# Kernel optimization log

Hardware: AMD Instinct MI355X
Metric: run time of the kernel (lower is better)

Reference implementation:

```python
import jax, jax.numpy as jnp
import numpy as np

N = 50000
E = 800000
IN_C, HID_C, OUT_C = 128, 128, 40
K = 3  # PyG TAGConv default number of hops


def setup_inputs() -> dict:
    key = jax.random.key(0)
    k1, k2, k3, k4, k5, k6, k7 = jax.random.split(key, 7)
    x = jax.random.normal(k1, (N, IN_C), dtype=jnp.float32)
    edge_index = jax.random.randint(k2, (2, E), 0, N, dtype=jnp.int64)
    # Linear((K+1)*in, out) weights (stored as [in_total, out] for x @ W)
    s1 = 1.0 / np.sqrt((K + 1) * IN_C)
    s2 = 1.0 / np.sqrt((K + 1) * HID_C)
    W1 = jax.random.uniform(k3, ((K + 1) * IN_C, HID_C), jnp.float32, -s1, s1)
    b1 = jax.random.uniform(k4, (HID_C,), jnp.float32, -s1, s1)
    W2 = jax.random.uniform(k5, ((K + 1) * HID_C, OUT_C), jnp.float32, -s2, s2)
    b2 = jax.random.uniform(k6, (OUT_C,), jnp.float32, -s2, s2)
    return {"x": x, "edge_index": edge_index, "W1": W1, "b1": b1, "W2": W2, "b2": b2}


def _sym_norm(src, dst):
    # GCN-style symmetric normalization: deg computed on destination (col)
    deg = jax.ops.segment_sum(jnp.ones((E,), jnp.float32), dst, num_segments=N)
    dis = jnp.where(deg > 0, jax.lax.rsqrt(jnp.maximum(deg, 1.0)), 0.0)
    return dis[src] * dis[dst]  # [E]


def _tag_layer(x, src, dst, norm, W, b):
    xs = [x]
    h = x
    for _ in range(K):
        h = jax.ops.segment_sum(h[src] * norm[:, None], dst, num_segments=N)
        xs.append(h)
    return jnp.concatenate(xs, axis=1) @ W + b


def reference(x, edge_index, W1, b1, W2, b2):
    src, dst = edge_index[0], edge_index[1]
    norm = _sym_norm(src, dst)
    h = jax.nn.relu(_tag_layer(x, src, dst, norm, W1, b1))
    # F.dropout(training=False) is identity at inference
    h = _tag_layer(h, src, dst, norm, W2, b2)
    return jax.nn.log_softmax(h, axis=1)
```

## Files before the change

kernel.cpp:

```cpp
#include <hip/hip_runtime.h>
#include <hip/hip_bf16.h>

#define NNODES 50000
#define NROWP  50176
#define NEDGES 800000
#define KHOP 3
#define SCAN_NB 49
#define NBKT 196
#define BCAP 6144
#define ABLK 400
#define ACH  2000

typedef __attribute__((ext_vector_type(8))) short short8v;
typedef __attribute__((ext_vector_type(8))) __bf16 bf16x8;
typedef __attribute__((ext_vector_type(4))) float f32x4;

__device__ inline unsigned short f2bf(float f) {
  unsigned u = __builtin_bit_cast(unsigned, f);
  u += 0x7fffu + ((u >> 16) & 1u);
  return (unsigned short)(u >> 16);
}
__device__ inline float bf2f(unsigned short h) {
  return __builtin_bit_cast(float, (unsigned)h << 16);
}
__device__ inline float bflo(unsigned u) { return __builtin_bit_cast(float, u << 16); }
__device__ inline float bfhi(unsigned u) { return __builtin_bit_cast(float, u & 0xffff0000u); }

__device__ inline void gload_lds16(const void* g, void* l) {
  __builtin_amdgcn_global_load_lds(
      (const __attribute__((address_space(1))) unsigned int*)g,
      (__attribute__((address_space(3))) unsigned int*)l, 16, 0, 0);
}

__device__ inline f32x4 mfma_bf16(bf16x8 a, bf16x8 b, f32x4 c) {
  return __builtin_amdgcn_mfma_f32_16x16x32_bf16(a, b, c, 0, 0, 0);
}

__device__ inline void fma8(float* acc, float w, short8v v) {
  uint4 u = __builtin_bit_cast(uint4, v);
  acc[0] = fmaf(w, bflo(u.x), acc[0]);
  acc[1] = fmaf(w, bfhi(u.x), acc[1]);
  acc[2] = fmaf(w, bflo(u.y), acc[2]);
  acc[3] = fmaf(w, bfhi(u.y), acc[3]);
  acc[4] = fmaf(w, bflo(u.z), acc[4]);
  acc[5] = fmaf(w, bfhi(u.z), acc[5]);
  acc[6] = fmaf(w, bflo(u.w), acc[6]);
  acc[7] = fmaf(w, bfhi(u.w), acc[7]);
}

__device__ inline void fma4(float* acc, float w, uint2 v) {
  acc[0] = fmaf(w, bflo(v.x), acc[0]);
  acc[1] = fmaf(w, bfhi(v.x), acc[1]);
  acc[2] = fmaf(w, bflo(v.y), acc[2]);
  acc[3] = fmaf(w, bfhi(v.y), acc[3]);
}

__global__ __launch_bounds__(256) void bucketA_kernel(
    const int* __restrict__ src, const int* __restrict__ dst,
    int* __restrict__ bcur, int2* __restrict__ bkt) {
  __shared__ int2 eb[ACH];
  __shared__ int hist[256];
  __shared__ int base[256];
  int tid = threadIdx.x;
  int e0 = blockIdx.x * ACH;
  int cnt = NEDGES - e0; if (cnt > ACH) cnt = ACH;
  hist[tid] = 0;
  __syncthreads();
  for (int i = tid; i < cnt; i += 256) {
    int s = src[e0 + i], d = dst[e0 + i];
    eb[i] = make_int2(s, d);
    atomicAdd(&hist[d >> 8], 1);
  }
  __syncthreads();
  base[tid] = atomicAdd(&bcur[tid], hist[tid]);
  hist[tid] = 0;
  __syncthreads();
  for (int i = tid; i < cnt; i += 256) {
    int2 e = eb[i];
    int b = e.y >> 8;
    int off = atomicAdd(&hist[b], 1);
    bkt[(size_t)b * BCAP + base[b] + off] = e;
  }
}

__global__ __launch_bounds__(256) void histB_kernel(
    const int* __restrict__ bcur, const int2* __restrict__ bkt,
    int* __restrict__ cnt, int n) {
  __shared__ int h[256];
  int b = blockIdx.x, tid = threadIdx.x;
  h[tid] = 0;
  __syncthreads();
  int sz = bcur[b];
  for (int i = tid; i < sz; i += 256)
    atomicAdd(&h[bkt[(size_t)b * BCAP + i].y & 255], 1);
  __syncthreads();
  int node = b * 256 + tid;
  if (node < n) cnt[node] = h[tid];
}

__global__ __launch_bounds__(256) void bsum_kernel(const int* __restrict__ cnt,
                                                   int* __restrict__ bsums, int n) {
  __shared__ int sd[256];
  int tid = threadIdx.x;
  int base = blockIdx.x * 1024 + tid * 4;
  int s = 0;
  if (base + 4 <= n) {
    int4 v = *(const int4*)&cnt[base];
    s = v.x + v.y + v.z + v.w;
  }
  sd[tid] = s;
  __syncthreads();
  for (int o = 128; o; o >>= 1) {
    if (tid < o) sd[tid] += sd[tid + o];
    __syncthreads();
  }
  if (tid == 0) bsums[blockIdx.x] = sd[0];
}

__global__ __launch_bounds__(64) void bscan_kernel(const int* __restrict__ bsums,
                                                   int* __restrict__ boff,
                                                   int* __restrict__ row_ptr,
                                                   int nb, int n) {
  int tid = threadIdx.x;
  int own = (tid < nb) ? bsums[tid] : 0;
  int v = own;
#pragma unroll
  for (int o = 1; o < 64; o <<= 1) {
    int t = __shfl_up(v, o, 64);
    if (tid >= o) v += t;
  }
  if (tid < nb) boff[tid] = v - own;
  if (tid == 63) row_ptr[n] = v;
}

__global__ __launch_bounds__(256) void bfinal_kernel(const int* __restrict__ cnt,
                                                     const int* __restrict__ boff,
                                                     int* __restrict__ row_ptr,
                                                     float* __restrict__ dis, int n) {
  __shared__ int sd[256];
  int tid = threadIdx.x;
  int base = blockIdx.x * 1024 + tid * 4;
  int4 v = make_int4(0, 0, 0, 0);
  bool ok = (base + 4 <= n);
  if (ok) v = *(const int4*)&cnt[base];
  int s = v.x + v.y + v.z + v.w;
  sd[tid] = s;
  __syncthreads();
  for (int o = 1; o < 256; o <<= 1) {
    int t = (tid >= o) ? sd[tid - o] : 0;
    __syncthreads();
    sd[tid] += t;
    __syncthreads();
  }
  if (ok) {
    int run = boff[blockIdx.x] + sd[tid] - s;
    int4 rp;
    rp.x = run;
    rp.y = run + v.x;
    rp.z = rp.y + v.y;
    rp.w = rp.z + v.z;
    *(int4*)&row_ptr[base] = rp;
    float4 dv;
    dv.x = (v.x > 0) ? rsqrtf((float)v.x) : 0.f;
    dv.y = (v.y > 0) ? rsqrtf((float)v.y) : 0.f;
    dv.z = (v.z > 0) ? rsqrtf((float)v.z) : 0.f;
    dv.w = (v.w > 0) ? rsqrtf((float)v.w) : 0.f;
    *(float4*)&dis[base] = dv;
  }
}

__global__ __launch_bounds__(256) void scatB_kernel(
    const int* __restrict__ bcur, const int2* __restrict__ bkt,
    const int* __restrict__ row_ptr, const float* __restrict__ dis,
    int2* __restrict__ csr, int n) {
  __shared__ int cur[256];
  int b = blockIdx.x, tid = threadIdx.x;
  int node = b * 256 + tid;
  cur[tid] = (node < n) ? row_ptr[node] : 0;
  __syncthreads();
  int sz = bcur[b];
  for (int i = tid; i < sz; i += 256) {
    int2 e = bkt[(size_t)b * BCAP + i];
    int pos = atomicAdd(&cur[e.y & 255], 1);
    int2 ent;
    ent.x = e.x;
    ent.y = __float_as_int(dis[e.x] * dis[e.y]);
    csr[pos] = ent;
  }
}

__global__ void wprep_kernel(const float* __restrict__ W1, const float* __restrict__ W2,
                             unsigned short* __restrict__ W1t,
                             unsigned short* __restrict__ W2pt) {
  int t = blockIdx.x * blockDim.x + threadIdx.x;
  if (t < 512 * 128) {
    int c = t >> 9, k = t & 511;
    W1t[t] = f2bf(W1[(size_t)k * 128 + c]);
  } else if (t < 512 * 128 + 160 * 128) {
    int u = t - 512 * 128;
    int q = u >> 7, r = u & 127;
    int k = q / 40, c = q - k * 40;
    W2pt[u] = f2bf(W2[(size_t)(k * 128 + r) * 40 + c]);
  }
}

__global__ void copyx_kernel(const float* __restrict__ x, unsigned short* __restrict__ P, int n) {
  int t = blockIdx.x * blockDim.x + threadIdx.x;
  int i = t >> 5;
  int c4 = (t & 31) << 2;
  if (i < n) {
    float4 v = *(const float4*)&x[(size_t)i * 128 + c4];
    unsigned lo = (unsigned)f2bf(v.x) | ((unsigned)f2bf(v.y) << 16);
    unsigned hi = (unsigned)f2bf(v.z) | ((unsigned)f2bf(v.w) << 16);
    uint2 o; o.x = lo; o.y = hi;
    *(uint2*)&P[(size_t)i * 512 + c4] = o;
  }
}

__global__ __launch_bounds__(256) void prop128c_kernel(
    const unsigned short* __restrict__ in, unsigned short* __restrict__ out,
    const int* __restrict__ row_ptr, const int2* __restrict__ csr, int n) {
  int node = (int)((blockIdx.x * blockDim.x + threadIdx.x) >> 6);
  int lane = threadIdx.x & 63;
  if (node >= n) return;
  int beg = row_ptr[node], end = row_ptr[node + 1];
  int deg = end - beg;
  int2 ent = make_int2(0, 0);
  if (lane < deg) ent = csr[beg + lane];
  const int grp = lane >> 4, sub = lane & 15;
  float acc[8] = {0.f, 0.f, 0.f, 0.f, 0.f, 0.f, 0.f, 0.f};
  int m = deg < 64 ? deg : 64;
  for (int j = 0; j < m; j += 4) {
    int idx = j + grp;
    bool act = idx < m;
    int ic = act ? idx : m - 1;
    int s = __shfl(ent.x, ic, 64);
    float w = __int_as_float(__shfl(ent.y, ic, 64));
    if (!act) w = 0.f;
    short8v v = *(const short8v*)(in + (size_t)s * 512 + sub * 8);
    fma8(acc, w, v);
  }
  for (int t = beg + 64; t < end; ++t) {
    int2 e0 = csr[t];
    float w = (grp == 0) ? __int_as_float(e0.y) : 0.f;
    short8v v = *(const short8v*)(in + (size_t)e0.x * 512 + sub * 8);
    fma8(acc, w, v);
  }
#pragma unroll
  for (int i = 0; i < 8; ++i) {
    acc[i] += __shfl_xor(acc[i], 16, 64);
    acc[i] += __shfl_xor(acc[i], 32, 64);
  }
  if (grp == 0) {
    uint4 r;
    r.x = (unsigned)f2bf(acc[0]) | ((unsigned)f2bf(acc[1]) << 16);
    r.y = (unsigned)f2bf(acc[2]) | ((unsigned)f2bf(acc[3]) << 16);
    r.z = (unsigned)f2bf(acc[4]) | ((unsigned)f2bf(acc[5]) << 16);
    r.w = (unsigned)f2bf(acc[6]) | ((unsigned)f2bf(acc[7]) << 16);
    *(uint4*)(out + (size_t)node * 512 + sub * 8) = r;
  }
}

__global__ __launch_bounds__(256) void gemm1m_kernel(
    const unsigned short* __restrict__ A,
    const unsigned short* __restrict__ Bt,
    const float* __restrict__ bias,
    unsigned short* __restrict__ H) {
  __shared__ short As[64 * 32];
  __shared__ short Bs[128 * 32];
  const int tid = threadIdx.x;
  const int lane = tid & 63;
  const int w = tid >> 6;
  const int wr = w & 1;
  const int wc = w >> 1;
  const int row0 = blockIdx.x * 64;
  f32x4 acc[2][4];
#pragma unroll
  for (int i = 0; i < 2; ++i)
#pragma unroll
    for (int j = 0; j < 4; ++j) acc[i][j] = (f32x4)0.f;

  const int lrow = lane >> 2;
  const int lkp = lane & 3;

  for (int k0 = 0; k0 < 512; k0 += 32) {
    gload_lds16(A + (size_t)(row0 + w * 16 + lrow) * 512 + k0 + lkp * 8, &As[w * 512]);
    gload_lds16(Bt + (size_t)(w * 16 + lrow) * 512 + k0 + lkp * 8, &Bs[w * 512]);
    gload_lds16(Bt + (size_t)((w + 4) * 16 + lrow) * 512 + k0 + lkp * 8, &Bs[(w + 4) * 512]);
    __syncthreads();
    const int kg = lane >> 4, rr = lane & 15;
    bf16x8 af[2], bfr[4];
#pragma unroll
    for (int mr = 0; mr < 2; ++mr)
      af[mr] = __builtin_bit_cast(bf16x8,
          *(const short8v*)&As[(wr * 32 + mr * 16 + rr) * 32 + kg * 8]);
#pragma unroll
    for (int nr = 0; nr < 4; ++nr)
      bfr[nr] = __builtin_bit_cast(bf16x8,
          *(const short8v*)&Bs[(wc * 64 + nr * 16 + rr) * 32 + kg * 8]);
#pragma unroll
    for (int mr = 0; mr < 2; ++mr)
#pragma unroll
      for (int nr = 0; nr < 4; ++nr)
        acc[mr][nr] = mfma_bf16(af[mr], bfr[nr], acc[mr][nr]);
    __syncthreads();
  }
  const int cg = lane >> 4, cl = lane & 15;
#pragma unroll
  for (int mr = 0; mr < 2; ++mr)
#pragma unroll
    for (int nr = 0; nr < 4; ++nr) {
      int col = wc * 64 + nr * 16 + cl;
      float bv = bias[col];
#pragma unroll
      for (int j = 0; j < 4; ++j) {
        int row = row0 + wr * 32 + mr * 16 + cg * 4 + j;
        H[(size_t)row * 128 + col] = f2bf(fmaxf(acc[mr][nr][j] + bv, 0.f));
      }
    }
}

__global__ __launch_bounds__(256) void gemm2m_kernel(
    const unsigned short* __restrict__ A,
    const unsigned short* __restrict__ Bt,
    unsigned short* __restrict__ G) {
  __shared__ short As[64 * 32];
  __shared__ short Bs[160 * 32];
  const int tid = threadIdx.x;
  const int lane = tid & 63;
  const int w = tid >> 6;
  const int row0 = blockIdx.x * 64;
  f32x4 acc[10];
#pragma unroll
  for (int i = 0; i < 10; ++i) acc[i] = (f32x4)0.f;
  const int lrow = lane >> 2, lkp = lane & 3;

  for (int k0 = 0; k0 < 128; k0 += 32) {
    gload_lds16(A + (size_t)(row0 + w * 16 + lrow) * 128 + k0 + lkp * 8, &As[w * 512]);
    for (int c = w; c < 10; c += 4)
      gload_lds16(Bt + (size_t)(c * 16 + lrow) * 128 + k0 + lkp * 8, &Bs[c * 512]);
    __syncthreads();
    const int kg = lane >> 4, rr = lane & 15;
    bf16x8 af = __builtin_bit_cast(bf16x8,
        *(const short8v*)&As[(w * 16 + rr) * 32 + kg * 8]);
#pragma unroll
    for (int nr = 0; nr < 10; ++nr) {
      bf16x8 bfr = __builtin_bit_cast(bf16x8,
          *(const short8v*)&Bs[(nr * 16 + rr) * 32 + kg * 8]);
      acc[nr] = mfma_bf16(af, bfr, acc[nr]);
    }
    __syncthreads();
  }
  const int cg = lane >> 4, cl = lane & 15;
#pragma unroll
  for (int nr = 0; nr < 10; ++nr) {
    int col = nr * 16 + cl;
    int k = col / 40;
    int o = col - k * 40;
#pragma unroll
    for (int j = 0; j < 4; ++j) {
      int row = row0 + w * 16 + cg * 4 + j;
      G[(size_t)k * NROWP * 64 + (size_t)row * 64 + o] = f2bf(acc[nr][j]);
    }
  }
}

__global__ __launch_bounds__(256) void prop40c_kernel(
    const unsigned short* __restrict__ in,
    const unsigned short* __restrict__ add,
    unsigned short* __restrict__ out,
    const int* __restrict__ row_ptr, const int2* __restrict__ csr, int n) {
  int node = (int)((blockIdx.x * blockDim.x + threadIdx.x) >> 6);
  int lane = threadIdx.x & 63;
  if (node >= n) return;
  int beg = row_ptr[node], end = row_ptr[node + 1];
  int deg = end - beg;
  int2 ent = make_int2(0, 0);
  if (lane < deg) ent = csr[beg + lane];
  const int grp = lane >> 4, sub = lane & 15;
  float acc[4] = {0.f, 0.f, 0.f, 0.f};
  if (grp == 0) {
    uint2 a = *(const uint2*)(add + (size_t)node * 64 + sub * 4);
    acc[0] = bflo(a.x); acc[1] = bfhi(a.x);
    acc[2] = bflo(a.y); acc[3] = bfhi(a.y);
  }
  int m = deg < 64 ? deg : 64;
  for (int j = 0; j < m; j += 4) {
    int idx = j + grp;
    bool act = idx < m;
    int ic = act ? idx : m - 1;
    int s = __shfl(ent.x, ic, 64);
    float w = __int_as_float(__shfl(ent.y, ic, 64));
    if (!act) w = 0.f;
    uint2 v = *(const uint2*)(in + (size_t)s * 64 + sub * 4);
    fma4(acc, w, v);
  }
  for (int t = beg + 64; t < end; ++t) {
    int2 e0 = csr[t];
    float w = (grp == 0) ? __int_as_float(e0.y) : 0.f;
    uint2 v = *(const uint2*)(in + (size_t)e0.x * 64 + sub * 4);
    fma4(acc, w, v);
  }
#pragma unroll
  for (int i = 0; i < 4; ++i) {
    acc[i] += __shfl_xor(acc[i], 16, 64);
    acc[i] += __shfl_xor(acc[i], 32, 64);
  }
  if (grp == 0) {
    uint2 r;
    r.x = (unsigned)f2bf(acc[0]) | ((unsigned)f2bf(acc[1]) << 16);
    r.y = (unsigned)f2bf(acc[2]) | ((unsigned)f2bf(acc[3]) << 16);
    *(uint2*)(out + (size_t)node * 64 + sub * 4) = r;
  }
}

__global__ __launch_bounds__(256) void prop40c_lsm_kernel(
    const unsigned short* __restrict__ in,
    const unsigned short* __restrict__ add,
    const float* __restrict__ b2,
    float* __restrict__ out,
    const int* __restrict__ row_ptr, const int2* __restrict__ csr, int n) {
  int node = (int)((blockIdx.x * blockDim.x + threadIdx.x) >> 6);
  int lane = threadIdx.x & 63;
  if (node >= n) return;
  int beg = row_ptr[node], end = row_ptr[node + 1];
  int deg = end - beg;
  int2 ent = make_int2(0, 0);
  if (lane < deg) ent = csr[beg + lane];
  const int grp = lane >> 4, sub = lane & 15;
  float acc[4] = {0.f, 0.f, 0.f, 0.f};
  if (grp == 0) {
    uint2 a = *(const uint2*)(add + (size_t)node * 64 + sub * 4);
    acc[0] = bflo(a.x); acc[1] = bfhi(a.x);
    acc[2] = bflo(a.y); acc[3] = bfhi(a.y);
  }
  int m = deg < 64 ? deg : 64;
  for (int j = 0; j < m; j += 4) {
    int idx = j + grp;
    bool act = idx < m;
    int ic = act ? idx : m - 1;
    int s = __shfl(ent.x, ic, 64);
    float w = __int_as_float(__shfl(ent.y, ic, 64));
    if (!act) w = 0.f;
    uint2 v = *(const uint2*)(in + (size_t)s * 64 + sub * 4);
    fma4(acc, w, v);
  }
  for (int t = beg + 64; t < end; ++t) {
    int2 e0 = csr[t];
    float w = (grp == 0) ? __int_as_float(e0.y) : 0.f;
    uint2 v = *(const uint2*)(in + (size_t)e0.x * 64 + sub * 4);
    fma4(acc, w, v);
  }
#pragma unroll
  for (int i = 0; i < 4; ++i) {
    acc[i] += __shfl_xor(acc[i], 16, 64);
    acc[i] += __shfl_xor(acc[i], 32, 64);
  }
  bool val = (sub < 10);
  float vv[4];
  if (val) {
    float4 bv = *(const float4*)(b2 + sub * 4);
    vv[0] = acc[0] + bv.x; vv[1] = acc[1] + bv.y;
    vv[2] = acc[2] + bv.z; vv[3] = acc[3] + bv.w;
  } else {
    vv[0] = vv[1] = vv[2] = vv[3] = -__builtin_inff();
  }
  float mx = fmaxf(fmaxf(vv[0], vv[1]), fmaxf(vv[2], vv[3]));
#pragma unroll
  for (int o = 1; o < 16; o <<= 1) mx = fmaxf(mx, __shfl_xor(mx, o, 64));
  float s = 0.f;
  if (val)
    s = expf(vv[0] - mx) + expf(vv[1] - mx) + expf(vv[2] - mx) + expf(vv[3] - mx);
#pragma unroll
  for (int o = 1; o < 16; o <<= 1) s += __shfl_xor(s, o, 64);
  if (val) {
    float ls = logf(s);
    float4 o4;
    o4.x = vv[0] - mx - ls; o4.y = vv[1] - mx - ls;
    o4.z = vv[2] - mx - ls; o4.w = vv[3] - mx - ls;
    *(float4*)(out + (size_t)node * 40 + sub * 4) = o4;
  }
}

extern "C" void kernel_launch(void* const* d_in, const int* in_sizes, int n_in,
                              void* d_out, int out_size, void* d_ws, size_t ws_size,
                              hipStream_t stream) {
  const float* x  = (const float*)d_in[0];
  const int*   ei = (const int*)d_in[1];
  const float* W1 = (const float*)d_in[2];
  const float* b1 = (const float*)d_in[3];
  const float* W2 = (const float*)d_in[4];
  const float* b2 = (const float*)d_in[5];
  const int* srcv = ei;
  const int* dstv = ei + NEDGES;
  float* out = (float*)d_out;

  char* wsb = (char*)d_ws;
  size_t off = 0;
  auto alloc = [&](size_t bytes) {
    char* p = wsb + off;
    off += (bytes + 255) & ~(size_t)255;
    return p;
  };
  int*            cnt     = (int*)            alloc((size_t)NNODES * 4);
  float*          dis     = (float*)          alloc((size_t)NNODES * 4);
  int*            row_ptr = (int*)            alloc(((size_t)NNODES + 1) * 4);
  int*            bcur    = (int*)            alloc((size_t)256 * 4);
  int*            bsums   = (int*)            alloc((size_t)SCAN_NB * 4);
  int*            boff    = (int*)            alloc((size_t)SCAN_NB * 4);
  int2*           bkt     = (int2*)           alloc((size_t)NBKT * BCAP * 8);
  int2*           csr     = (int2*)           alloc((size_t)NEDGES * 8);
  unsigned short* W1t     = (unsigned short*) alloc((size_t)128 * 512 * 2);
  unsigned short* W2pt    = (unsigned short*) alloc((size_t)160 * 128 * 2);
  unsigned short* P       = (unsigned short*) alloc((size_t)NROWP * 512 * 2);
  unsigned short* H       = (unsigned short*) alloc((size_t)NROWP * 128 * 2);
  unsigned short* G       = (unsigned short*) alloc((size_t)4 * NROWP * 64 * 2);
  unsigned short* tb      = (unsigned short*) alloc((size_t)NNODES * 64 * 2);
  unsigned short* t2      = (unsigned short*) alloc((size_t)NNODES * 64 * 2);

  unsigned short* G0 = G;
  unsigned short* G1 = G + (size_t)1 * NROWP * 64;
  unsigned short* G2 = G + (size_t)2 * NROWP * 64;
  unsigned short* G3 = G + (size_t)3 * NROWP * 64;

  hipMemsetAsync(bcur, 0, 256 * 4, stream);
  bucketA_kernel<<<ABLK, 256, 0, stream>>>(srcv, dstv, bcur, bkt);
  histB_kernel<<<NBKT, 256, 0, stream>>>(bcur, bkt, cnt, NNODES);
  bsum_kernel<<<SCAN_NB, 256, 0, stream>>>(cnt, bsums, NNODES);
  bscan_kernel<<<1, 64, 0, stream>>>(bsums, boff, row_ptr, SCAN_NB, NNODES);
  bfinal_kernel<<<SCAN_NB, 256, 0, stream>>>(cnt, boff, row_ptr, dis, NNODES);
  scatB_kernel<<<NBKT, 256, 0, stream>>>(bcur, bkt, row_ptr, dis, csr, NNODES);
  wprep_kernel<<<(512 * 128 + 160 * 128 + 255) / 256, 256, 0, stream>>>(W1, W2, W1t, W2pt);
  copyx_kernel<<<((NNODES * 32) + 255) / 256, 256, 0, stream>>>(x, P, NNODES);

  const int prop_blocks = (NNODES * 64 + 255) / 256;
  for (int k = 1; k <= KHOP; ++k)
    prop128c_kernel<<<prop_blocks, 256, 0, stream>>>(P + 128 * (k - 1), P + 128 * k,
                                                     row_ptr, csr, NNODES);
  const int gemm_blocks = (NNODES + 63) / 64;
  gemm1m_kernel<<<gemm_blocks, 256, 0, stream>>>(P, W1t, b1, H);
  gemm2m_kernel<<<gemm_blocks, 256, 0, stream>>>(H, W2pt, G);
  prop40c_kernel<<<prop_blocks, 256, 0, stream>>>(G3, G2, tb, row_ptr, csr, NNODES);
  prop40c_kernel<<<prop_blocks, 256, 0, stream>>>(tb, G1, t2, row_ptr, csr, NNODES);
  prop40c_lsm_kernel<<<prop_blocks, 256, 0, stream>>>(t2, G0, b2, out, row_ptr, csr, NNODES);
}
```

Before: 254.3 us.

## Split feature matrix into 32-column blocks and map column blocks to XCDs in propagation

Changes the P buffer from row-major 512-wide rows to a blocked layout of 32 bf16 columns per node per block. Each workgroup in the 128-wide propagation now handles one 32-column block for 4 nodes, and the workgroup id is decoded so that each column block lands on a fixed pair of XCDs. The goal is for each XCD's L2 to cache only its slice of the gathered features, which cuts cross-XCD cache duplication in the random neighbor gathers. In exchange there are 4x more workgroups, each doing smaller 8-byte loads, and the neighbor lists are re-read once per column block. The copy and GEMM1 A-operand loads are adapted to the new layout.

```diff
diff --git a/kernel.cpp b/kernel.cpp
--- a/kernel.cpp
+++ b/kernel.cpp
@@ -10,6 +10,7 @@
 #define BCAP 6144
 #define ABLK 400
 #define ACH  2000
+#define PXWG 50000
 
 typedef __attribute__((ext_vector_type(8))) short short8v;
 typedef __attribute__((ext_vector_type(8))) __bf16 bf16x8;
@@ -20,9 +21,6 @@
   u += 0x7fffu + ((u >> 16) & 1u);
   return (unsigned short)(u >> 16);
 }
-__device__ inline float bf2f(unsigned short h) {
-  return __builtin_bit_cast(float, (unsigned)h << 16);
-}
 __device__ inline float bflo(unsigned u) { return __builtin_bit_cast(float, u << 16); }
 __device__ inline float bfhi(unsigned u) { return __builtin_bit_cast(float, u & 0xffff0000u); }
 
@@ -34,18 +32,6 @@
 
 __device__ inline f32x4 mfma_bf16(bf16x8 a, bf16x8 b, f32x4 c) {
   return __builtin_amdgcn_mfma_f32_16x16x32_bf16(a, b, c, 0, 0, 0);
-}
-
-__device__ inline void fma8(float* acc, float w, short8v v) {
-  uint4 u = __builtin_bit_cast(uint4, v);
-  acc[0] = fmaf(w, bflo(u.x), acc[0]);
-  acc[1] = fmaf(w, bfhi(u.x), acc[1]);
-  acc[2] = fmaf(w, bflo(u.y), acc[2]);
-  acc[3] = fmaf(w, bfhi(u.y), acc[3]);
-  acc[4] = fmaf(w, bflo(u.z), acc[4]);
-  acc[5] = fmaf(w, bfhi(u.z), acc[5]);
-  acc[6] = fmaf(w, bflo(u.w), acc[6]);
-  acc[7] = fmaf(w, bfhi(u.w), acc[7]);
 }
 
 __device__ inline void fma4(float* acc, float w, uint2 v) {
@@ -204,60 +190,68 @@
   }
 }
 
-__global__ void copyx_kernel(const float* __restrict__ x, unsigned short* __restrict__ P, int n) {
+__global__ void copyx_kernel(const float* __restrict__ x, unsigned short* __restrict__ Pb, int n) {
   int t = blockIdx.x * blockDim.x + threadIdx.x;
-  int i = t >> 5;
-  int c4 = (t & 31) << 2;
+  int i = t >> 4;
+  int sl = t & 15;
   if (i < n) {
-    float4 v = *(const float4*)&x[(size_t)i * 128 + c4];
-    unsigned lo = (unsigned)f2bf(v.x) | ((unsigned)f2bf(v.y) << 16);
-    unsigned hi = (unsigned)f2bf(v.z) | ((unsigned)f2bf(v.w) << 16);
-    uint2 o; o.x = lo; o.y = hi;
-    *(uint2*)&P[(size_t)i * 512 + c4] = o;
-  }
-}
-
-__global__ __launch_bounds__(256) void prop128c_kernel(
+    int c = sl >> 2, q = sl & 3;
+    float4 v0 = *(const float4*)&x[(size_t)i * 128 + c * 32 + q * 8];
+    float4 v1 = *(const float4*)&x[(size_t)i * 128 + c * 32 + q * 8 + 4];
+    uint4 r;
+    r.x = (unsigned)f2bf(v0.x) | ((unsigned)f2bf(v0.y) << 16);
+    r.y = (unsigned)f2bf(v0.z) | ((unsigned)f2bf(v0.w) << 16);
+    r.z = (unsigned)f2bf(v1.x) | ((unsigned)f2bf(v1.y) << 16);
+    r.w = (unsigned)f2bf(v1.z) | ((unsigned)f2bf(v1.w) << 16);
+    *(uint4*)(Pb + ((size_t)c * NROWP + i) * 32 + q * 8) = r;
+  }
+}
+
+__global__ __launch_bounds__(256) void prop128x_kernel(
     const unsigned short* __restrict__ in, unsigned short* __restrict__ out,
     const int* __restrict__ row_ptr, const int2* __restrict__ csr, int n) {
-  int node = (int)((blockIdx.x * blockDim.x + threadIdx.x) >> 6);
+  int wgid = blockIdx.x;
+  int xcd = wgid & 7;
+  int cb = xcd >> 1;
+  int chunk = (wgid >> 3) * 2 + (xcd & 1);
+  int node = chunk * 4 + (threadIdx.x >> 6);
   int lane = threadIdx.x & 63;
   if (node >= n) return;
   int beg = row_ptr[node], end = row_ptr[node + 1];
   int deg = end - beg;
   int2 ent = make_int2(0, 0);
   if (lane < deg) ent = csr[beg + lane];
-  const int grp = lane >> 4, sub = lane & 15;
-  float acc[8] = {0.f, 0.f, 0.f, 0.f, 0.f, 0.f, 0.f, 0.f};
+  const int slot = lane >> 3, sub = lane & 7;
+  const unsigned short* inb = in + (size_t)cb * NROWP * 32;
+  float acc[4] = {0.f, 0.f, 0.f, 0.f};
   int m = deg < 64 ? deg : 64;
-  for (int j = 0; j < m; j += 4) {
-    int idx = j + grp;
+  for (int j = 0; j < m; j += 8) {
+    int idx = j + slot;
     bool act = idx < m;
     int ic = act ? idx : m - 1;
     int s = __shfl(ent.x, ic, 64);
     float w = __int_as_float(__shfl(ent.y, ic, 64));
     if (!act) w = 0.f;
-    short8v v = *(const short8v*)(in + (size_t)s * 512 + sub * 8);
-    fma8(acc, w, v);
+    uint2 v = *(const uint2*)(inb + (size_t)s * 32 + sub * 4);
+    fma4(acc, w, v);
   }
   for (int t = beg + 64; t < end; ++t) {
     int2 e0 = csr[t];
-    float w = (grp == 0) ? __int_as_float(e0.y) : 0.f;
-    short8v v = *(const short8v*)(in + (size_t)e0.x * 512 + sub * 8);
-    fma8(acc, w, v);
-  }
-#pragma unroll
-  for (int i = 0; i < 8; ++i) {
+    float w = (slot == 0) ? __int_as_float(e0.y) : 0.f;
+    uint2 v = *(const uint2*)(inb + (size_t)e0.x * 32 + sub * 4);
+    fma4(acc, w, v);
+  }
+#pragma unroll
+  for (int i = 0; i < 4; ++i) {
+    acc[i] += __shfl_xor(acc[i], 8, 64);
     acc[i] += __shfl_xor(acc[i], 16, 64);
     acc[i] += __shfl_xor(acc[i], 32, 64);
   }
-  if (grp == 0) {
-    uint4 r;
+  if (slot == 0) {
+    uint2 r;
     r.x = (unsigned)f2bf(acc[0]) | ((unsigned)f2bf(acc[1]) << 16);
     r.y = (unsigned)f2bf(acc[2]) | ((unsigned)f2bf(acc[3]) << 16);
-    r.z = (unsigned)f2bf(acc[4]) | ((unsigned)f2bf(acc[5]) << 16);
-    r.w = (unsigned)f2bf(acc[6]) | ((unsigned)f2bf(acc[7]) << 16);
-    *(uint4*)(out + (size_t)node * 512 + sub * 8) = r;
+    *(uint2*)(out + ((size_t)cb * NROWP + node) * 32 + sub * 4) = r;
   }
 }
 
@@ -284,7 +278,8 @@
   const int lkp = lane & 3;
 
   for (int k0 = 0; k0 < 512; k0 += 32) {
-    gload_lds16(A + (size_t)(row0 + w * 16 + lrow) * 512 + k0 + lkp * 8, &As[w * 512]);
+    const int blk = k0 >> 5;
+    gload_lds16(A + ((size_t)blk * NROWP + row0 + w * 16 + lrow) * 32 + lkp * 8, &As[w * 512]);
     gload_lds16(Bt + (size_t)(w * 16 + lrow) * 512 + k0 + lkp * 8, &Bs[w * 512]);
     gload_lds16(Bt + (size_t)((w + 4) * 16 + lrow) * 512 + k0 + lkp * 8, &Bs[(w + 4) * 512]);
     __syncthreads();
@@ -531,15 +526,16 @@
   bfinal_kernel<<<SCAN_NB, 256, 0, stream>>>(cnt, boff, row_ptr, dis, NNODES);
   scatB_kernel<<<NBKT, 256, 0, stream>>>(bcur, bkt, row_ptr, dis, csr, NNODES);
   wprep_kernel<<<(512 * 128 + 160 * 128 + 255) / 256, 256, 0, stream>>>(W1, W2, W1t, W2pt);
-  copyx_kernel<<<((NNODES * 32) + 255) / 256, 256, 0, stream>>>(x, P, NNODES);
-
-  const int prop_blocks = (NNODES * 64 + 255) / 256;
+  copyx_kernel<<<((NNODES * 16) + 255) / 256, 256, 0, stream>>>(x, P, NNODES);
+
+  const size_t hopstride = (size_t)4 * NROWP * 32;
   for (int k = 1; k <= KHOP; ++k)
-    prop128c_kernel<<<prop_blocks, 256, 0, stream>>>(P + 128 * (k - 1), P + 128 * k,
-                                                     row_ptr, csr, NNODES);
+    prop128x_kernel<<<PXWG, 256, 0, stream>>>(P + hopstride * (k - 1), P + hopstride * k,
+                                              row_ptr, csr, NNODES);
   const int gemm_blocks = (NNODES + 63) / 64;
   gemm1m_kernel<<<gemm_blocks, 256, 0, stream>>>(P, W1t, b1, H);
   gemm2m_kernel<<<gemm_blocks, 256, 0, stream>>>(H, W2pt, G);
+  const int prop_blocks = (NNODES * 64 + 255) / 256;
   prop40c_kernel<<<prop_blocks, 256, 0, stream>>>(G3, G2, tb, row_ptr, csr, NNODES);
   prop40c_kernel<<<prop_blocks, 256, 0, stream>>>(tb, G1, t2, row_ptr, csr, NNODES);
   prop40c_lsm_kernel<<<prop_blocks, 256, 0, stream>>>(t2, G0, b2, out, row_ptr, csr, NNODES);
```

New measurement: 332.7 us. 1.31x slower.
